# Kernel tuning notes

Measured on AMD Instinct MI355X. Metric: run time of the kernel, lower is better.

Reference implementation:

```python
import jax, jax.numpy as jnp
import numpy as np

D = 1024
H = 16
HD = D // H  # 64
S = 2048
B = 1


def setup_inputs() -> dict:
    key = jax.random.key(0)
    ks = jax.random.split(key, 6)
    return {
        "GLO": jax.random.normal(ks[0], (B, S, D), dtype=jnp.float32),
        "LOC": jax.random.normal(ks[1], (B, S, D), dtype=jnp.float32),
        "W_q": jax.random.normal(ks[2], (H, D, HD), dtype=jnp.float32),
        "W_k": jax.random.normal(ks[3], (H, D, HD), dtype=jnp.float32),
        "W_v": jax.random.normal(ks[4], (H, D, HD), dtype=jnp.float32),
        "W_o": jax.random.normal(ks[5], (H * HD, D), dtype=jnp.float32),
    }


def _cross_attn(q_src, kv_src, W_q, W_k, W_v, W_o):
    # q_src: [B,Sq,D], kv_src: [B,Sk,D]
    b, sq, _ = q_src.shape
    Q = jnp.einsum('bsd,hde->bhse', q_src, W_q)   # [B,H,Sq,hd]
    K = jnp.einsum('bsd,hde->bhse', kv_src, W_k)  # [B,H,Sk,hd]
    V = jnp.einsum('bsd,hde->bhse', kv_src, W_v)  # [B,H,Sk,hd]
    scores = jnp.einsum('bhqe,bhke->bhqk', Q, K) / jnp.sqrt(jnp.float32(HD))
    weights = jax.nn.softmax(scores, axis=-1)
    out = jnp.einsum('bhqk,bhke->bhqe', weights, V)  # [B,H,Sq,hd]
    # Faithful to torch .view (raw memory reinterpretation, no head transpose)
    out = out.reshape(b, sq, H * HD)
    return out @ W_o  # [B,Sq,D]


def reference(GLO, LOC, W_q, W_k, W_v, W_o):
    GLO_prime = _cross_attn(GLO, LOC, W_q, W_k, W_v, W_o)
    LOC_prime = _cross_attn(LOC, GLO, W_q, W_k, W_v, W_o)
    return (GLO_prime, LOC_prime)
```

## Files before the change

### kernel.cpp

```cpp
#include <hip/hip_runtime.h>
#include <math.h>

#define S_LEN 2048
#define D_DIM 1024
#define NH 16
#define HD 64

typedef __attribute__((ext_vector_type(8))) short bf16x8;
typedef __attribute__((ext_vector_type(4))) float f32x4;

#define MFMA(a, b, c) __builtin_amdgcn_mfma_f32_16x16x32_bf16((a), (b), (c), 0, 0, 0)

__device__ __forceinline__ unsigned short f2bf(float x) {
    unsigned int u = __float_as_uint(x);
    u = (u + 0x7FFFu + ((u >> 16) & 1u)) >> 16;
    return (unsigned short)u;
}
__device__ __forceinline__ float bf2f(unsigned short b) {
    return __uint_as_float(((unsigned int)b) << 16);
}
__device__ __forceinline__ void gl_lds16(const void* g, void* l) {
    __builtin_amdgcn_global_load_lds((const __attribute__((address_space(1))) unsigned int*)g,
                                     (__attribute__((address_space(3))) unsigned int*)l, 16, 0, 0);
}


__global__ __launch_bounds__(256) void prep(const float* __restrict__ GLO,
                                            const float* __restrict__ LOC,
                                            const float* __restrict__ Wq,
                                            const float* __restrict__ Wk,
                                            const float* __restrict__ Wv,
                                            const float* __restrict__ Wo,
                                            unsigned short* __restrict__ Xh,
                                            unsigned short* __restrict__ Xl,
                                            unsigned short* __restrict__ Wqh,
                                            unsigned short* __restrict__ Wql,
                                            unsigned short* __restrict__ Wkh,
                                            unsigned short* __restrict__ Wkl,
                                            unsigned short* __restrict__ Wvt,
                                            unsigned short* __restrict__ Wot) {
    int idx = blockIdx.x * 256 + threadIdx.x;
    if (idx < (1 << 22)) {
        const float* src = (idx & (1 << 21)) ? LOC : GLO;
        float x = src[idx & ((1 << 21) - 1)];
        int r = idx >> 10;
        int k = idx & 1023;
        size_t t = (size_t)(r >> 7) * 131072 + (size_t)(k >> 6) * 8192 + (r & 127) * 64 +
                   ((((k >> 3) & 7) ^ (r & 7)) * 8) + (k & 7);
        unsigned short h = f2bf(x);
        Xh[t] = h;
        Xl[t] = f2bf(x - bf2f(h));
    } else {
        idx -= (1 << 22);
        int sec = idx >> 20;
        int i = idx & 0xFFFFF;
        if (sec < 3) {
            int e = i & 63;
            int d = (i >> 6) & 1023;
            int h = i >> 16;
            float wv = ((sec == 0) ? Wq : (sec == 1) ? Wk : Wv)[h * 65536 + d * 64 + e];
            size_t t = (size_t)h * 65536 + (size_t)(d >> 6) * 4096 + e * 64 +
                       ((((d >> 3) & 7) ^ (e & 7)) * 8) + (d & 7);
            if (sec == 0) {
                wv *= 0.18033688011112042f;
                unsigned short hi = f2bf(wv);
                Wqh[t] = hi;
                Wql[t] = f2bf(wv - bf2f(hi));
            } else if (sec == 1) {
                unsigned short hi = f2bf(wv);
                Wkh[t] = hi;
                Wkl[t] = f2bf(wv - bf2f(hi));
            } else {
                Wvt[t] = f2bf(wv);
            }
        } else {
            int n = i & 1023;
            int k = i >> 10;
            size_t t = (size_t)(n >> 6) * 65536 + (size_t)(k >> 6) * 4096 + (n & 63) * 64 +
                       ((((k >> 3) & 7) ^ (n & 7)) * 8) + (k & 7);
            Wot[t] = f2bf(Wo[k * 1024 + n]);
        }
    }
}

__global__ __launch_bounds__(256) void qkv_proj(const unsigned short* __restrict__ Xh,
                                                const unsigned short* __restrict__ Xl,
                                                const unsigned short* __restrict__ Wqh,
                                                const unsigned short* __restrict__ Wql,
                                                const unsigned short* __restrict__ Wkh,
                                                const unsigned short* __restrict__ Wkl,
                                                const unsigned short* __restrict__ Wvt,
                                                unsigned short* __restrict__ Qh,
                                                unsigned short* __restrict__ Ql,
                                                unsigned short* __restrict__ Kh,
                                                unsigned short* __restrict__ Kl,
                                                unsigned short* __restrict__ Vt) {
    __shared__ unsigned short lds[36864];
    const int bid = blockIdx.x;
    const int mblk = bid & 31;
    const int head = bid >> 5;
    const int tid = threadIdx.x;
    const int lane = tid & 63;
    const int w = tid >> 6;
    const int l15 = lane & 15, quad = lane >> 4;

    f32x4 aq[2][4] = {}, ak[2][4] = {}, av[2][4] = {};
    const size_t abase0 = (size_t)mblk * 131072;
    const size_t bbase0 = (size_t)head * 65536;

    for (int kb = 0; kb < 16; ++kb) {
        __syncthreads();
        {
            const size_t ab = abase0 + (size_t)kb * 8192;
            const size_t bb = bbase0 + (size_t)kb * 4096;
#pragma unroll
            for (int j = 0; j < 4; ++j) {
                int seg = j * 256 + tid;
                gl_lds16(Xh + ab + seg * 8, &lds[seg * 8]);
                gl_lds16(Xl + ab + seg * 8, &lds[8192 + seg * 8]);
            }
#pragma unroll
            for (int j = 0; j < 2; ++j) {
                int seg = j * 256 + tid;
                gl_lds16(Wqh + bb + seg * 8, &lds[16384 + seg * 8]);
                gl_lds16(Wql + bb + seg * 8, &lds[20480 + seg * 8]);
                gl_lds16(Wkh + bb + seg * 8, &lds[24576 + seg * 8]);
                gl_lds16(Wkl + bb + seg * 8, &lds[28672 + seg * 8]);
                gl_lds16(Wvt + bb + seg * 8, &lds[32768 + seg * 8]);
            }
        }
        __syncthreads();

#pragma unroll
        for (int ksub = 0; ksub < 2; ++ksub) {
            bf16x8 ah[2], al8[2];
#pragma unroll
            for (int mt = 0; mt < 2; ++mt) {
                int row = w * 32 + mt * 16 + l15;
                int g = (ksub * 4 + quad) ^ (row & 7);
                ah[mt] = *(const bf16x8*)&lds[row * 64 + g * 8];
                al8[mt] = *(const bf16x8*)&lds[8192 + row * 64 + g * 8];
            }
#pragma unroll
            for (int nt = 0; nt < 4; ++nt) {
                int col = nt * 16 + l15;
                int o = col * 64 + ((ksub * 4 + quad) ^ (col & 7)) * 8;
                bf16x8 bqh = *(const bf16x8*)&lds[16384 + o];
                bf16x8 bql = *(const bf16x8*)&lds[20480 + o];
                bf16x8 bkh = *(const bf16x8*)&lds[24576 + o];
                bf16x8 bkl = *(const bf16x8*)&lds[28672 + o];
                bf16x8 bv = *(const bf16x8*)&lds[32768 + o];
#pragma unroll
                for (int mt = 0; mt < 2; ++mt) {
                    f32x4 a = aq[mt][nt];
                    a = MFMA(ah[mt], bqh, a);
                    a = MFMA(ah[mt], bql, a);
                    a = MFMA(al8[mt], bqh, a);
                    aq[mt][nt] = a;
                    f32x4 b = ak[mt][nt];
                    b = MFMA(ah[mt], bkh, b);
                    b = MFMA(ah[mt], bkl, b);
                    b = MFMA(al8[mt], bkh, b);
                    ak[mt][nt] = b;
                    av[mt][nt] = MFMA(ah[mt], bv, av[mt][nt]);
                }
            }
        }
    }

#pragma unroll
    for (int mt = 0; mt < 2; ++mt) {
        const int rbase = mblk * 128 + w * 32 + mt * 16 + quad * 4;
#pragma unroll
        for (int nt = 0; nt < 4; ++nt) {
            const int col = head * 64 + nt * 16 + l15;
#pragma unroll
            for (int r = 0; r < 4; ++r) {
                size_t a = (size_t)(rbase + r) * D_DIM + col;
                float vq = aq[mt][nt][r];
                unsigned short hq = f2bf(vq);
                Qh[a] = hq;
                Ql[a] = f2bf(vq - bf2f(hq));
                float vk = ak[mt][nt][r];
                unsigned short hk = f2bf(vk);
                Kh[a] = hk;
                Kl[a] = f2bf(vk - bf2f(hk));
            }
            ushort4 vp;
            vp.x = f2bf(av[mt][nt][0]);
            vp.y = f2bf(av[mt][nt][1]);
            vp.z = f2bf(av[mt][nt][2]);
            vp.w = f2bf(av[mt][nt][3]);
            *(ushort4*)(Vt + (size_t)col * (2 * S_LEN) + rbase) = vp;
        }
    }
}

__global__ __launch_bounds__(256) void attn_kernel(const unsigned short* __restrict__ Qh_,
                                                   const unsigned short* __restrict__ Ql_,
                                                   const unsigned short* __restrict__ Kh_,
                                                   const unsigned short* __restrict__ Kl_,
                                                   const unsigned short* __restrict__ Vt_,
                                                   unsigned short* __restrict__ Oatt) {
    __shared__ unsigned short lds[28672];
    const int bid = blockIdx.x;
    const int qblk = bid & 15;
    const int head = (bid >> 4) & 15;
    const int dir = bid >> 8;
    const int src_q = dir, src_kv = 1 - dir;

    const int tid = threadIdx.x;
    const int lane = tid & 63;
    const int w = tid >> 6;
    const int l15 = lane & 15, quad = lane >> 4;
    const int q0w = qblk * 128 + w * 32;

    const unsigned short* KhB0 = Kh_ + (size_t)(src_kv * S_LEN) * D_DIM + head * 64;
    const unsigned short* KlB0 = Kl_ + (size_t)(src_kv * S_LEN) * D_DIM + head * 64;
    const unsigned short* Vtp = Vt_ + (size_t)(head * 64) * (2 * S_LEN) + src_kv * S_LEN;

    const int i0 = tid, i1 = 256 + tid;
    const int sr0 = i0 >> 3, sc0 = ((i0 & 7) ^ (sr0 & 7)) * 8;
    const int sr1 = i1 >> 3, sc1 = ((i1 & 7) ^ (sr1 & 7)) * 8;

    auto stage = [&](int k0, int boff) {
        const unsigned short* KhB = KhB0 + (size_t)k0 * D_DIM;
        const unsigned short* KlB = KlB0 + (size_t)k0 * D_DIM;
        const unsigned short* VB = Vtp + k0;
        gl_lds16(KhB + (size_t)sr0 * D_DIM + sc0, &lds[boff + i0 * 8]);
        gl_lds16(KhB + (size_t)sr1 * D_DIM + sc1, &lds[boff + i1 * 8]);
        gl_lds16(KlB + (size_t)sr0 * D_DIM + sc0, &lds[boff + 4096 + i0 * 8]);
        gl_lds16(KlB + (size_t)sr1 * D_DIM + sc1, &lds[boff + 4096 + i1 * 8]);
        gl_lds16(VB + (size_t)sr0 * (2 * S_LEN) + sc0, &lds[boff + 8192 + i0 * 8]);
        gl_lds16(VB + (size_t)sr1 * (2 * S_LEN) + sc1, &lds[boff + 8192 + i1 * 8]);
    };

    bf16x8 qh[2][2], ql[2][2];
#pragma unroll
    for (int mt = 0; mt < 2; ++mt) {
        const size_t qrow =
            (size_t)(src_q * S_LEN + q0w + mt * 16 + l15) * D_DIM + head * 64 + quad * 8;
#pragma unroll
        for (int c = 0; c < 2; ++c) {
            qh[mt][c] = *(const bf16x8*)(Qh_ + qrow + c * 32);
            ql[mt][c] = *(const bf16x8*)(Ql_ + qrow + c * 32);
        }
    }

    f32x4 o[2][4] = {};
    float mi[2] = {-1e30f, -1e30f}, li[2] = {0.f, 0.f};
    unsigned short* Pw = lds + 24576 + w * 1024;

    auto chunk = [&](int kb) {
        f32x4 sa[2][4];
#pragma unroll
        for (int kt = 0; kt < 4; ++kt) {
            const int row = kt * 16 + l15;
            const int s0 = (quad ^ (row & 7)) * 8;
            const int s1 = ((4 + quad) ^ (row & 7)) * 8;
            bf16x8 kh0 = *(const bf16x8*)&lds[kb + row * 64 + s0];
            bf16x8 kh1 = *(const bf16x8*)&lds[kb + row * 64 + s1];
            bf16x8 kl0 = *(const bf16x8*)&lds[kb + 4096 + row * 64 + s0];
            bf16x8 kl1 = *(const bf16x8*)&lds[kb + 4096 + row * 64 + s1];
#pragma unroll
            for (int mt = 0; mt < 2; ++mt) {
                f32x4 a = {};
                a = MFMA(kh0, qh[mt][0], a);
                a = MFMA(kh1, qh[mt][1], a);
                a = MFMA(kl0, qh[mt][0], a);
                a = MFMA(kl1, qh[mt][1], a);
                a = MFMA(kh0, ql[mt][0], a);
                a = MFMA(kh1, ql[mt][1], a);
                sa[mt][kt] = a;
            }
        }

#pragma unroll
        for (int mt = 0; mt < 2; ++mt) {
            f32x4 t4 = __builtin_elementwise_max(__builtin_elementwise_max(sa[mt][0], sa[mt][1]),
                                                 __builtin_elementwise_max(sa[mt][2], sa[mt][3]));
            float tm = fmaxf(fmaxf(t4[0], t4[1]), fmaxf(t4[2], t4[3]));
            tm = fmaxf(tm, __shfl_xor(tm, 16, 64));
            tm = fmaxf(tm, __shfl_xor(tm, 32, 64));
            if (__ballot(tm > mi[mt])) {
                float mn = fmaxf(mi[mt], tm);
                float al = exp2f(mi[mt] - mn);
                mi[mt] = mn;
                li[mt] *= al;
                const f32x4 alv = {al, al, al, al};
#pragma unroll
                for (int et = 0; et < 4; ++et) o[mt][et] *= alv;
            }
            const float mn = mi[mt];
            const f32x4 mnv = {mn, mn, mn, mn};
            f32x4 rs4 = {};
#pragma unroll
            for (int kt = 0; kt < 4; ++kt) {
                f32x4 p = sa[mt][kt] - mnv;
#pragma unroll
                for (int r = 0; r < 4; ++r) p[r] = exp2f(p[r]);
                rs4 += p;
                unsigned u0 = __float_as_uint(p[0]) + 0x8000u;
                unsigned u1 = __float_as_uint(p[1]) + 0x8000u;
                unsigned u2 = __float_as_uint(p[2]) + 0x8000u;
                unsigned u3 = __float_as_uint(p[3]) + 0x8000u;
                uint2 pk;
                pk.x = __builtin_amdgcn_perm(u1, u0, 0x07060302u);
                pk.y = __builtin_amdgcn_perm(u3, u2, 0x07060302u);
                int g = (kt * 2 + (quad >> 1)) ^ (l15 & 7);
                *(uint2*)&Pw[l15 * 64 + g * 8 + (quad & 1) * 4] = pk;
            }
            float rs = (rs4[0] + rs4[1]) + (rs4[2] + rs4[3]);
            rs += __shfl_xor(rs, 16, 64);
            rs += __shfl_xor(rs, 32, 64);
            li[mt] += rs;

#pragma unroll
            for (int c = 0; c < 2; ++c) {
                bf16x8 pf = *(const bf16x8*)&Pw[l15 * 64 + (((c * 4 + quad) ^ (l15 & 7)) * 8)];
#pragma unroll
                for (int et = 0; et < 4; ++et) {
                    const int row = et * 16 + l15;
                    const int sl = ((c * 4 + quad) ^ (row & 7)) * 8;
                    bf16x8 vf = *(const bf16x8*)&lds[kb + 8192 + row * 64 + sl];
                    o[mt][et] = MFMA(vf, pf, o[mt][et]);
                }
            }
        }
    };

    stage(0, 0);
#pragma unroll 1
    for (int kd = 0; kd < 32; kd += 2) {
        __syncthreads();
        if (kd + 1 < 32) stage((kd + 1) * 64, 12288);
        chunk(0);
        __syncthreads();
        if (kd + 2 < 32) stage((kd + 2) * 64, 0);
        chunk(12288);
    }

    const size_t obase = (size_t)(dir * 16 + head) * 131072 + (size_t)l15 * 8192;
#pragma unroll
    for (int mt = 0; mt < 2; ++mt) {
        float rl = __builtin_amdgcn_rcpf(li[mt]);
        const int rowit = qblk * 8 + w * 2 + mt;
#pragma unroll
        for (int et = 0; et < 4; ++et) {
            int g = ((et * 2 + (quad >> 1)) ^ (rowit & 7)) & 7;
            ushort4 pk;
            pk.x = f2bf(o[mt][et][0] * rl);
            pk.y = f2bf(o[mt][et][1] * rl);
            pk.z = f2bf(o[mt][et][2] * rl);
            pk.w = f2bf(o[mt][et][3] * rl);
            *(ushort4*)(Oatt + obase + (size_t)rowit * 64 + g * 8 + (quad & 1) * 4) = pk;
        }
    }
}

__global__ __launch_bounds__(256) void oproj(const unsigned short* __restrict__ Oatt,
                                             const unsigned short* __restrict__ Wot,
                                             float* __restrict__ out) {
    __shared__ unsigned short lds[12288];
    const int bid = blockIdx.x;
    const int nblk = bid & 15;
    const int mblk = bid >> 4;
    const int tid = threadIdx.x;
    const int lane = tid & 63, w = tid >> 6, l15 = lane & 15, quad = lane >> 4;

    f32x4 acc[2][4] = {};
    const size_t abase = (size_t)mblk * 131072;
    const size_t bbase = (size_t)nblk * 65536;
    for (int kb = 0; kb < 16; ++kb) {
        __syncthreads();
#pragma unroll
        for (int j = 0; j < 4; ++j) {
            int seg = j * 256 + tid;
            gl_lds16(Oatt + abase + (size_t)kb * 8192 + seg * 8, &lds[seg * 8]);
        }
#pragma unroll
        for (int j = 0; j < 2; ++j) {
            int seg = j * 256 + tid;
            gl_lds16(Wot + bbase + (size_t)kb * 4096 + seg * 8, &lds[8192 + seg * 8]);
        }
        __syncthreads();
#pragma unroll
        for (int ksub = 0; ksub < 2; ++ksub) {
            bf16x8 a[2];
#pragma unroll
            for (int mt = 0; mt < 2; ++mt) {
                int row = w * 32 + mt * 16 + l15;
                a[mt] = *(const bf16x8*)&lds[row * 64 + (((ksub * 4 + quad) ^ (row & 7)) * 8)];
            }
#pragma unroll
            for (int nt = 0; nt < 4; ++nt) {
                int col = nt * 16 + l15;
                bf16x8 b =
                    *(const bf16x8*)&lds[8192 + col * 64 + (((ksub * 4 + quad) ^ (col & 7)) * 8)];
#pragma unroll
                for (int mt = 0; mt < 2; ++mt) acc[mt][nt] = MFMA(a[mt], b, acc[mt][nt]);
            }
        }
    }
#pragma unroll
    for (int mt = 0; mt < 2; ++mt) {
        const int rbase = mblk * 128 + w * 32 + mt * 16 + quad * 4;
#pragma unroll
        for (int nt = 0; nt < 4; ++nt)
#pragma unroll
            for (int r = 0; r < 4; ++r)
                out[(size_t)(rbase + r) * D_DIM + nblk * 64 + nt * 16 + l15] = acc[mt][nt][r];
    }
}

extern "C" void kernel_launch(void* const* d_in, const int* in_sizes, int n_in, void* d_out,
                              int out_size, void* d_ws, size_t ws_size, hipStream_t stream) {
    const float* GLO = (const float*)d_in[0];
    const float* LOC = (const float*)d_in[1];
    const float* Wq = (const float*)d_in[2];
    const float* Wk = (const float*)d_in[3];
    const float* Wv = (const float*)d_in[4];
    const float* Wo = (const float*)d_in[5];
    float* out = (float*)d_out;

    unsigned short* ws = (unsigned short*)d_ws;
    unsigned short* Xh = ws + 0;
    unsigned short* Xl = ws + 4194304;
    unsigned short* Wqh = ws + 8388608;
    unsigned short* Wql = ws + 9437184;
    unsigned short* Wkh = ws + 10485760;
    unsigned short* Wkl = ws + 11534336;
    unsigned short* Wvt = ws + 12582912;
    unsigned short* Wot = ws + 13631488;
    unsigned short* Qh = ws + 14680064;
    unsigned short* Ql = ws + 18874368;
    unsigned short* Kh = ws + 23068672;
    unsigned short* Kl = ws + 27262976;
    unsigned short* Vt = ws + 31457280;
    unsigned short* Oatt = ws + 35651584;

    prep<<<32768, 256, 0, stream>>>(GLO, LOC, Wq, Wk, Wv, Wo, Xh, Xl, Wqh, Wql, Wkh, Wkl, Wvt, Wot);
    qkv_proj<<<512, 256, 0, stream>>>(Xh, Xl, Wqh, Wql, Wkh, Wkl, Wvt, Qh, Ql, Kh, Kl, Vt);
    attn_kernel<<<512, 256, 0, stream>>>(Qh, Ql, Kh, Kl, Vt, Oatt);
    oproj<<<512, 256, 0, stream>>>(Oatt, Wot, out);
}
```

Measured before the change: 277.4 us.

## Double-buffer oproj LDS loads and defer softmax row-sum reduction

The output-projection kernel now uses two LDS buffers, so the global-to-LDS load of the next K-slice overlaps the MFMA work on the current one, instead of a load-sync-compute sequence each iteration. The attention kernel keeps per-lane partial row sums and reduces them across lanes only once at the end, which removes two shuffles per chunk. It also skips a whole chunk when every score is more than 64 (log2 units) below the running max, on the basis that its contribution underflows. LDS use in oproj doubles, and the skip is an approximation that could drop tiny probability mass.

```diff
diff --git a/kernel.cpp b/kernel.cpp
--- a/kernel.cpp
+++ b/kernel.cpp
@@ -248,7 +248,8 @@
     }
 
     f32x4 o[2][4] = {};
-    float mi[2] = {-1e30f, -1e30f}, li[2] = {0.f, 0.f};
+    float mi[2] = {-1e30f, -1e30f};
+    float lip[2] = {0.f, 0.f};
     unsigned short* Pw = lds + 24576 + w * 1024;
 
     auto chunk = [&](int kb) {
@@ -282,11 +283,12 @@
             float tm = fmaxf(fmaxf(t4[0], t4[1]), fmaxf(t4[2], t4[3]));
             tm = fmaxf(tm, __shfl_xor(tm, 16, 64));
             tm = fmaxf(tm, __shfl_xor(tm, 32, 64));
+            if (!__ballot(tm > mi[mt] - 64.f)) continue;
             if (__ballot(tm > mi[mt])) {
                 float mn = fmaxf(mi[mt], tm);
                 float al = exp2f(mi[mt] - mn);
                 mi[mt] = mn;
-                li[mt] *= al;
+                lip[mt] *= al;
                 const f32x4 alv = {al, al, al, al};
 #pragma unroll
                 for (int et = 0; et < 4; ++et) o[mt][et] *= alv;
@@ -310,10 +312,7 @@
                 int g = (kt * 2 + (quad >> 1)) ^ (l15 & 7);
                 *(uint2*)&Pw[l15 * 64 + g * 8 + (quad & 1) * 4] = pk;
             }
-            float rs = (rs4[0] + rs4[1]) + (rs4[2] + rs4[3]);
-            rs += __shfl_xor(rs, 16, 64);
-            rs += __shfl_xor(rs, 32, 64);
-            li[mt] += rs;
+            lip[mt] += (rs4[0] + rs4[1]) + (rs4[2] + rs4[3]);
 
 #pragma unroll
             for (int c = 0; c < 2; ++c) {
@@ -343,7 +342,10 @@
     const size_t obase = (size_t)(dir * 16 + head) * 131072 + (size_t)l15 * 8192;
 #pragma unroll
     for (int mt = 0; mt < 2; ++mt) {
-        float rl = __builtin_amdgcn_rcpf(li[mt]);
+        float lq = lip[mt];
+        lq += __shfl_xor(lq, 16, 64);
+        lq += __shfl_xor(lq, 32, 64);
+        float rl = __builtin_amdgcn_rcpf(lq);
         const int rowit = qblk * 8 + w * 2 + mt;
 #pragma unroll
         for (int et = 0; et < 4; ++et) {
@@ -361,7 +363,7 @@
 __global__ __launch_bounds__(256) void oproj(const unsigned short* __restrict__ Oatt,
                                              const unsigned short* __restrict__ Wot,
                                              float* __restrict__ out) {
-    __shared__ unsigned short lds[12288];
+    __shared__ unsigned short lds[24576];
     const int bid = blockIdx.x;
     const int nblk = bid & 15;
     const int mblk = bid >> 4;
@@ -371,37 +373,52 @@
     f32x4 acc[2][4] = {};
     const size_t abase = (size_t)mblk * 131072;
     const size_t bbase = (size_t)nblk * 65536;
-    for (int kb = 0; kb < 16; ++kb) {
-        __syncthreads();
+
+    auto ostage = [&](int kb, int boff) {
 #pragma unroll
         for (int j = 0; j < 4; ++j) {
             int seg = j * 256 + tid;
-            gl_lds16(Oatt + abase + (size_t)kb * 8192 + seg * 8, &lds[seg * 8]);
+            gl_lds16(Oatt + abase + (size_t)kb * 8192 + seg * 8, &lds[boff + seg * 8]);
         }
 #pragma unroll
         for (int j = 0; j < 2; ++j) {
             int seg = j * 256 + tid;
-            gl_lds16(Wot + bbase + (size_t)kb * 4096 + seg * 8, &lds[8192 + seg * 8]);
-        }
-        __syncthreads();
+            gl_lds16(Wot + bbase + (size_t)kb * 4096 + seg * 8, &lds[boff + 8192 + seg * 8]);
+        }
+    };
+
+    auto compute = [&](int boff) {
 #pragma unroll
         for (int ksub = 0; ksub < 2; ++ksub) {
             bf16x8 a[2];
 #pragma unroll
             for (int mt = 0; mt < 2; ++mt) {
                 int row = w * 32 + mt * 16 + l15;
-                a[mt] = *(const bf16x8*)&lds[row * 64 + (((ksub * 4 + quad) ^ (row & 7)) * 8)];
+                a[mt] =
+                    *(const bf16x8*)&lds[boff + row * 64 + (((ksub * 4 + quad) ^ (row & 7)) * 8)];
             }
 #pragma unroll
             for (int nt = 0; nt < 4; ++nt) {
                 int col = nt * 16 + l15;
-                bf16x8 b =
-                    *(const bf16x8*)&lds[8192 + col * 64 + (((ksub * 4 + quad) ^ (col & 7)) * 8)];
+                bf16x8 b = *(const bf16x8*)&lds[boff + 8192 + col * 64 +
+                                                (((ksub * 4 + quad) ^ (col & 7)) * 8)];
 #pragma unroll
                 for (int mt = 0; mt < 2; ++mt) acc[mt][nt] = MFMA(a[mt], b, acc[mt][nt]);
             }
         }
-    }
+    };
+
+    ostage(0, 0);
+#pragma unroll 1
+    for (int kb = 0; kb < 16; kb += 2) {
+        __syncthreads();
+        if (kb + 1 < 16) ostage(kb + 1, 12288);
+        compute(0);
+        __syncthreads();
+        if (kb + 2 < 16) ostage(kb + 2, 0);
+        compute(12288);
+    }
+
 #pragma unroll
     for (int mt = 0; mt < 2; ++mt) {
         const int rbase = mblk * 128 + w * 32 + mt * 16 + quad * 4;
```

Result: no change. 280.9 us (+1.3%).
